# Kernel optimization log

Measured on AMD Instinct MI355X. Metric: run time of the kernel, lower is better.

Reference implementation:

```python
import jax, jax.numpy as jnp
import numpy as np

N_NODES = 50000
N_EDGES = 625000
DIM = 128
DROPOUT_P = 0.5


def setup_inputs() -> dict:
    key = jax.random.key(0)
    kx, ke, kw, kb = jax.random.split(key, 4)
    x = jax.random.normal(kx, (N_NODES, DIM), dtype=jnp.float32)
    edge_index = jax.random.randint(ke, (2, N_EDGES), 0, N_NODES, dtype=jnp.int64)
    # GCNConv linear weight (glorot-ish) and bias
    W = jax.random.normal(kw, (DIM, DIM), dtype=jnp.float32) / np.sqrt(DIM)
    b = jnp.zeros((DIM,), dtype=jnp.float32)
    return {"x": x, "edge_index": edge_index, "W": W, "b": b}


def reference(x, edge_index, W, b):
    N = x.shape[0]
    # --- add self-loops ---
    loop = jnp.arange(N, dtype=edge_index.dtype)
    src = jnp.concatenate([edge_index[0], loop])  # [E+N]
    dst = jnp.concatenate([edge_index[1], loop])  # [E+N]
    # --- symmetric normalization: deg computed on destination nodes ---
    deg = jax.ops.segment_sum(jnp.ones_like(src, dtype=x.dtype), dst, num_segments=N)
    dis = jnp.where(deg > 0, jax.lax.rsqrt(jnp.where(deg > 0, deg, 1.0)), 0.0)
    norm = dis[src] * dis[dst]  # [E+N]
    # --- linear transform, gather, scatter-add ---
    h = x @ W  # [N, D]
    msg = h[src] * norm[:, None]  # [E+N, D]
    out = jax.ops.segment_sum(msg, dst, num_segments=N) + b  # [N, D]
    # --- ReLU + dropout (training mode, fixed key) + residual ---
    out = jax.nn.relu(out)
    keep = jax.random.bernoulli(jax.random.key(42), 1.0 - DROPOUT_P, out.shape)
    out = jnp.where(keep, out / (1.0 - DROPOUT_P), 0.0)
    out = out + x  # residual: input_dim == output_dim
    return out
```

## Files before the change

### kernel.cpp

```cpp
#include <hip/hip_runtime.h>
#include <hip/hip_bf16.h>
#include <stdint.h>

#define NDIM 128
#define LDK 136
#define BSH 9
#define NB_A 1024
#define BCAP 9216

typedef __attribute__((ext_vector_type(8))) short bf16x8;
typedef __attribute__((ext_vector_type(4))) float f32x4;

__device__ __forceinline__ unsigned short f2bf(float f) {
    unsigned u = __float_as_uint(f);
    unsigned r = u + 0x7fffu + ((u >> 16) & 1u);
    return (unsigned short)(r >> 16);
}
__device__ __forceinline__ float bf2f(unsigned short s) {
    return __uint_as_float(((unsigned)s) << 16);
}

__device__ __forceinline__ void load_edge(const unsigned* __restrict__ w, int is64, int E,
                                          int e, int& s, int& d) {
    if (is64) {
        s = (int)w[(size_t)2 * e];
        d = (int)w[(size_t)2 * E + (size_t)2 * e];
    } else {
        s = (int)w[e];
        d = (int)w[(size_t)E + e];
    }
}

__global__ void detect_kernel(const unsigned* __restrict__ w, int* flag) {
    __shared__ int any_nonzero;
    if (threadIdx.x == 0) any_nonzero = 0;
    __syncthreads();
    int nz = 0;
    for (int k = threadIdx.x; k < 2048; k += 256) {
        if (w[2 * k + 1] != 0u) nz = 1;
    }
    if (nz) atomicOr(&any_nonzero, 1);
    __syncthreads();
    if (threadIdx.x == 0) *flag = any_nonzero ? 0 : 1;
}

__global__ __launch_bounds__(256) void hist_kernel(const unsigned* __restrict__ w,
                                                   const int* __restrict__ flag,
                                                   int* __restrict__ hist,
                                                   int E, int nbuck, int chunk) {
    __shared__ int h[128];
    int t = threadIdx.x;
    if (t < 128) h[t] = 0;
    __syncthreads();
    int is64 = *flag;
    int lo = blockIdx.x * chunk;
    int hi = lo + chunk; if (hi > E) hi = E;
    for (int e = lo + t; e < hi; e += 256) {
        int s, d; load_edge(w, is64, E, e, s, d);
        atomicAdd(&h[d >> BSH], 1);
    }
    __syncthreads();
    if (t < nbuck) hist[(size_t)t * gridDim.x + blockIdx.x] = h[t];
}

__global__ __launch_bounds__(1024) void scanhist_kernel(int* __restrict__ hist,
                                                        int* __restrict__ btot, int NB) {
    __shared__ int s[1024];
    int t = threadIdx.x;
    size_t base = (size_t)blockIdx.x * NB;
    int v = hist[base + t];
    s[t] = v;
    __syncthreads();
    for (int d = 1; d < 1024; d <<= 1) {
        int add = (t >= d) ? s[t - d] : 0;
        __syncthreads();
        s[t] += add;
        __syncthreads();
    }
    hist[base + t] = s[t] - v;
    if (t == 1023) btot[blockIdx.x] = s[1023];
}

__global__ __launch_bounds__(128) void scanbuck_kernel(const int* __restrict__ btot,
                                                       int* __restrict__ bbase, int nbuck,
                                                       int* __restrict__ off, int N, int E) {
    __shared__ int s[128];
    int t = threadIdx.x;
    int v = (t < nbuck) ? btot[t] : 0;
    s[t] = v;
    __syncthreads();
    for (int d = 1; d < 128; d <<= 1) {
        int add = (t >= d) ? s[t - d] : 0;
        __syncthreads();
        s[t] += add;
        __syncthreads();
    }
    if (t < nbuck) bbase[t] = s[t] - v;
    if (t == 0) off[N] = E;
}

__global__ __launch_bounds__(256) void bucket_kernel(const unsigned* __restrict__ w,
                                                     const int* __restrict__ flag,
                                                     const int* __restrict__ hist,
                                                     const int* __restrict__ bbase,
                                                     unsigned* __restrict__ ebuf,
                                                     int E, int nbuck, int chunk) {
    __shared__ int cur[128];
    int t = threadIdx.x;
    if (t < nbuck) cur[t] = bbase[t] + hist[(size_t)t * gridDim.x + blockIdx.x];
    __syncthreads();
    int is64 = *flag;
    int lo = blockIdx.x * chunk;
    int hi = lo + chunk; if (hi > E) hi = E;
    for (int e = lo + t; e < hi; e += 256) {
        int s, d; load_edge(w, is64, E, e, s, d);
        int b = d >> BSH;
        int p = atomicAdd(&cur[b], 1);
        ebuf[p] = ((unsigned)s << BSH) | (unsigned)(d & ((1 << BSH) - 1));
    }
}

__global__ __launch_bounds__(512) void csr_kernel(const unsigned* __restrict__ ebuf,
                                                  const int* __restrict__ bbase,
                                                  const int* __restrict__ btot,
                                                  int* __restrict__ adj,
                                                  int* __restrict__ off,
                                                  float* __restrict__ dis,
                                                  int N) {
    __shared__ int lcnt[512];
    __shared__ int lscan[512];
    __shared__ int cur[512];
    __shared__ int tile[BCAP];
    int b = blockIdx.x, t = threadIdx.x;
    int start = bbase[b], cnt = btot[b];
    lcnt[t] = 0;
    __syncthreads();
    for (int i = t; i < cnt; i += 512) atomicAdd(&lcnt[ebuf[start + i] & 511], 1);
    __syncthreads();
    int v = lcnt[t];
    lscan[t] = v;
    __syncthreads();
    for (int d = 1; d < 512; d <<= 1) {
        int add = (t >= d) ? lscan[t - d] : 0;
        __syncthreads();
        lscan[t] += add;
        __syncthreads();
    }
    int ex = lscan[t] - v;
    int node = (b << BSH) + t;
    if (node < N) {
        off[node] = start + ex;
        dis[node] = rsqrtf((float)(v + 1));
    }
    cur[t] = ex;
    __syncthreads();
    if (cnt <= BCAP) {
        for (int i = t; i < cnt; i += 512) {
            unsigned wo = ebuf[start + i];
            int p = atomicAdd(&cur[wo & 511], 1);
            tile[p] = (int)(wo >> BSH);
        }
        __syncthreads();
        for (int i = t; i < cnt; i += 512) adj[start + i] = tile[i];
    } else {
        for (int i = t; i < cnt; i += 512) {
            unsigned wo = ebuf[start + i];
            int p = atomicAdd(&cur[wo & 511], 1);
            adj[start + p] = (int)(wo >> BSH);
        }
    }
}

__global__ __launch_bounds__(256) void gemm_kernel(const float* __restrict__ x,
                                                   const float* __restrict__ W,
                                                   const float* __restrict__ dis,
                                                   unsigned short* __restrict__ hp,
                                                   int N, int ntiles) {
    __shared__ unsigned short Wt[NDIM][LDK];
    int tid = threadIdx.x;
    for (int i = tid; i < NDIM * NDIM; i += 256) {
        int k = i >> 7, c = i & 127;
        Wt[c][k] = f2bf(W[i]);
    }
    __syncthreads();

    const int lane = tid & 63;
    const int wv = tid >> 6;
    const int l15 = lane & 15;
    const int kg = lane >> 4;

    for (int tile = blockIdx.x; tile < ntiles; tile += gridDim.x) {
        const int rowbase = tile * 64 + wv * 16;
        const int arow = rowbase + l15;

        bf16x8 a[4];
#pragma unroll
        for (int s = 0; s < 4; ++s) {
            bf16x8 tt;
            if (arow < N) {
                const float* p = x + (size_t)arow * NDIM + s * 32 + kg * 8;
                float4 f0 = *(const float4*)p;
                float4 f1 = *(const float4*)(p + 4);
                tt[0] = (short)f2bf(f0.x); tt[1] = (short)f2bf(f0.y);
                tt[2] = (short)f2bf(f0.z); tt[3] = (short)f2bf(f0.w);
                tt[4] = (short)f2bf(f1.x); tt[5] = (short)f2bf(f1.y);
                tt[6] = (short)f2bf(f1.z); tt[7] = (short)f2bf(f1.w);
            } else {
#pragma unroll
                for (int e = 0; e < 8; ++e) tt[e] = 0;
            }
            a[s] = tt;
        }

        f32x4 acc[8];
#pragma unroll
        for (int ct = 0; ct < 8; ++ct) acc[ct] = (f32x4){0.f, 0.f, 0.f, 0.f};

#pragma unroll
        for (int ct = 0; ct < 8; ++ct) {
#pragma unroll
            for (int s = 0; s < 4; ++s) {
                bf16x8 bb = *(const bf16x8*)&Wt[ct * 16 + l15][s * 32 + kg * 8];
                acc[ct] = __builtin_amdgcn_mfma_f32_16x16x32_bf16(a[s], bb, acc[ct], 0, 0, 0);
            }
        }

        const int r0 = rowbase + kg * 4;
        float dv[4];
#pragma unroll
        for (int j = 0; j < 4; ++j) dv[j] = (r0 + j < N) ? dis[r0 + j] : 0.f;
#pragma unroll
        for (int ct = 0; ct < 8; ++ct) {
            int col = ct * 16 + l15;
#pragma unroll
            for (int j = 0; j < 4; ++j) {
                int r = r0 + j;
                if (r < N) hp[(size_t)r * NDIM + col] = f2bf(acc[ct][j] * dv[j]);
            }
        }
    }
}

__device__ __forceinline__ unsigned rotl32(unsigned v, int d) {
    return (v << d) | (v >> (32 - d));
}
__device__ __forceinline__ unsigned tf_bits(unsigned ctr) {
    unsigned x0 = 0u, x1 = ctr;
    const unsigned ks0 = 0u, ks1 = 42u, ks2 = 0u ^ 42u ^ 0x1BD11BDAu;
    x0 += ks0; x1 += ks1;
#define RND(r) { x0 += x1; x1 = rotl32(x1, (r)); x1 ^= x0; }
    RND(13) RND(15) RND(26) RND(6)   x0 += ks1; x1 += ks2 + 1u;
    RND(17) RND(29) RND(16) RND(24)  x0 += ks2; x1 += ks0 + 2u;
    RND(13) RND(15) RND(26) RND(6)   x0 += ks0; x1 += ks1 + 3u;
    RND(17) RND(29) RND(16) RND(24)  x0 += ks1; x1 += ks2 + 4u;
    RND(13) RND(15) RND(26) RND(6)   x0 += ks2; x1 += ks0 + 5u;
#undef RND
    return x0 ^ x1;
}

__global__ __launch_bounds__(256) void gather_kernel(const unsigned short* __restrict__ hp,
                                                     const float* __restrict__ x,
                                                     const int* __restrict__ off,
                                                     const int* __restrict__ adj,
                                                     const float* __restrict__ dis,
                                                     const float* __restrict__ b,
                                                     float* __restrict__ out, int N) {
    int wid = (int)((blockIdx.x * 256u + threadIdx.x) >> 6);
    int lane = threadIdx.x & 63;
    int half = lane >> 5;
    int l32 = lane & 31;
    int node = wid * 2 + half;
    bool valid = node < N;
    int nodec = valid ? node : N - 1;
    const float dn = dis[nodec];
    const int c0 = l32 * 4;
    const unsigned short* hpc = hp + c0;

    unsigned ctr = (unsigned)(nodec * NDIM + c0);
    unsigned bt0 = tf_bits(ctr);
    unsigned bt1 = tf_bits(ctr + 1u);
    unsigned bt2 = tf_bits(ctr + 2u);
    unsigned bt3 = tf_bits(ctr + 3u);

    uint2 hv = *(const uint2*)(hpc + (size_t)nodec * NDIM);
    float a00 = bf2f((unsigned short)hv.x), a01 = bf2f((unsigned short)(hv.x >> 16));
    float a02 = bf2f((unsigned short)hv.y), a03 = bf2f((unsigned short)(hv.y >> 16));
    float a10 = 0.f, a11 = 0.f, a12 = 0.f, a13 = 0.f;
    float a20 = 0.f, a21 = 0.f, a22 = 0.f, a23 = 0.f;
    float a30 = 0.f, a31 = 0.f, a32 = 0.f, a33 = 0.f;

    int k0 = valid ? off[nodec] : 0;
    int k1 = valid ? off[nodec + 1] : 0;
    int kb = k0;
    const int sbase = half << 5;
    while (kb < k1) {
        int nb = k1 - kb; if (nb > 32) nb = 32;
        int myadj = (kb + l32 < k1) ? adj[kb + l32] : 0;
        int j = 0;
        for (; j + 4 <= nb; j += 4) {
            int s0 = __shfl(myadj, sbase + j);
            int s1 = __shfl(myadj, sbase + j + 1);
            int s2 = __shfl(myadj, sbase + j + 2);
            int s3 = __shfl(myadj, sbase + j + 3);
            uint2 v0 = *(const uint2*)(hpc + (size_t)s0 * NDIM);
            uint2 v1 = *(const uint2*)(hpc + (size_t)s1 * NDIM);
            uint2 v2 = *(const uint2*)(hpc + (size_t)s2 * NDIM);
            uint2 v3 = *(const uint2*)(hpc + (size_t)s3 * NDIM);
            a00 += bf2f((unsigned short)v0.x); a01 += bf2f((unsigned short)(v0.x >> 16));
            a02 += bf2f((unsigned short)v0.y); a03 += bf2f((unsigned short)(v0.y >> 16));
            a10 += bf2f((unsigned short)v1.x); a11 += bf2f((unsigned short)(v1.x >> 16));
            a12 += bf2f((unsigned short)v1.y); a13 += bf2f((unsigned short)(v1.y >> 16));
            a20 += bf2f((unsigned short)v2.x); a21 += bf2f((unsigned short)(v2.x >> 16));
            a22 += bf2f((unsigned short)v2.y); a23 += bf2f((unsigned short)(v2.y >> 16));
            a30 += bf2f((unsigned short)v3.x); a31 += bf2f((unsigned short)(v3.x >> 16));
            a32 += bf2f((unsigned short)v3.y); a33 += bf2f((unsigned short)(v3.y >> 16));
        }
        for (; j < nb; ++j) {
            int s = __shfl(myadj, sbase + j);
            uint2 v = *(const uint2*)(hpc + (size_t)s * NDIM);
            a00 += bf2f((unsigned short)v.x); a01 += bf2f((unsigned short)(v.x >> 16));
            a02 += bf2f((unsigned short)v.y); a03 += bf2f((unsigned short)(v.y >> 16));
        }
        kb += nb;
    }

    float c0s = (a00 + a10) + (a20 + a30);
    float c1s = (a01 + a11) + (a21 + a31);
    float c2s = (a02 + a12) + (a22 + a32);
    float c3s = (a03 + a13) + (a23 + a33);

    float4 bb = *(const float4*)(b + c0);
    float v0 = fmaxf(fmaf(dn, c0s, bb.x), 0.f);
    float v1 = fmaxf(fmaf(dn, c1s, bb.y), 0.f);
    float v2 = fmaxf(fmaf(dn, c2s, bb.z), 0.f);
    float v3 = fmaxf(fmaf(dn, c3s, bb.w), 0.f);

    v0 = (bt0 >> 31) ? 0.f : v0 * 2.f;
    v1 = (bt1 >> 31) ? 0.f : v1 * 2.f;
    v2 = (bt2 >> 31) ? 0.f : v2 * 2.f;
    v3 = (bt3 >> 31) ? 0.f : v3 * 2.f;

    if (valid) {
        float4 xr = *(const float4*)(x + (size_t)node * NDIM + c0);
        float4 o;
        o.x = v0 + xr.x; o.y = v1 + xr.y; o.z = v2 + xr.z; o.w = v3 + xr.w;
        *(float4*)(out + (size_t)node * NDIM + c0) = o;
    }
}

extern "C" void kernel_launch(void* const* d_in, const int* in_sizes, int n_in,
                              void* d_out, int out_size, void* d_ws, size_t ws_size,
                              hipStream_t stream) {
    const float* x = (const float*)d_in[0];
    const unsigned* edge_w = (const unsigned*)d_in[1];
    const float* W = (const float*)d_in[2];
    const float* b = (const float*)d_in[3];
    float* out = (float*)d_out;

    const int N = in_sizes[0] / NDIM;
    const int E = in_sizes[1] / 2;
    const int nbuck = (N + (1 << BSH) - 1) >> BSH;
    const int chunk = (E + NB_A - 1) / NB_A;
    const int ntiles = (N + 63) / 64;

    char* ws = (char*)d_ws;
    unsigned short* hp = (unsigned short*)ws;
    float* dis   = (float*)(ws + (size_t)N * NDIM * sizeof(short));
    int*   off   = (int*)((char*)dis + (size_t)N * sizeof(float));
    int*   adj   = (int*)((char*)off + (size_t)(N + 4) * sizeof(int));
    unsigned* ebuf = (unsigned*)((char*)adj + (size_t)E * sizeof(int));
    int*   hist  = (int*)((char*)ebuf + (size_t)E * sizeof(unsigned));
    int*   btot  = (int*)((char*)hist + (size_t)128 * NB_A * sizeof(int));
    int*   bbase = (int*)((char*)btot + (size_t)128 * sizeof(int));
    int*   flag  = (int*)((char*)bbase + (size_t)128 * sizeof(int));

    detect_kernel<<<1, 256, 0, stream>>>(edge_w, flag);
    hist_kernel<<<NB_A, 256, 0, stream>>>(edge_w, flag, hist, E, nbuck, chunk);
    scanhist_kernel<<<nbuck, 1024, 0, stream>>>(hist, btot, NB_A);
    scanbuck_kernel<<<1, 128, 0, stream>>>(btot, bbase, nbuck, off, N, E);
    bucket_kernel<<<NB_A, 256, 0, stream>>>(edge_w, flag, hist, bbase, ebuf, E, nbuck, chunk);
    csr_kernel<<<nbuck, 512, 0, stream>>>(ebuf, bbase, btot, adj, off, dis, N);

    gemm_kernel<<<391, 256, 0, stream>>>(x, W, dis, hp, N, ntiles);

    int waves = (N + 1) / 2;
    gather_kernel<<<(waves + 3) / 4, 256, 0, stream>>>(hp, x, off, adj, dis, b, out, N);
}
```

Measured before the change: 84.65 us.

## Fuse detect and bucket-scan kernels, pre-convert W, unroll gather by eight

```diff
diff --git a/kernel.cpp b/kernel.cpp
--- a/kernel.cpp
+++ b/kernel.cpp
@@ -31,30 +31,37 @@
     }
 }
 
-__global__ void detect_kernel(const unsigned* __restrict__ w, int* flag) {
-    __shared__ int any_nonzero;
-    if (threadIdx.x == 0) any_nonzero = 0;
-    __syncthreads();
-    int nz = 0;
-    for (int k = threadIdx.x; k < 2048; k += 256) {
-        if (w[2 * k + 1] != 0u) nz = 1;
-    }
-    if (nz) atomicOr(&any_nonzero, 1);
-    __syncthreads();
-    if (threadIdx.x == 0) *flag = any_nonzero ? 0 : 1;
+__device__ __forceinline__ int detect_is64(const unsigned* __restrict__ w,
+                                           int lo, int hi, int E, int t, int* nzflag) {
+    if (t == 0) *nzflag = 0;
+    __syncthreads();
+    int k = lo + t;
+    if (k < hi && w[2 * (size_t)k + 1] != 0u) atomicOr(nzflag, 1);
+    __syncthreads();
+    return *nzflag ? 0 : 1;
 }
 
 __global__ __launch_bounds__(256) void hist_kernel(const unsigned* __restrict__ w,
-                                                   const int* __restrict__ flag,
+                                                   const float* __restrict__ W,
+                                                   unsigned short* __restrict__ WbfT,
                                                    int* __restrict__ hist,
+                                                   int* __restrict__ lock,
                                                    int E, int nbuck, int chunk) {
     __shared__ int h[128];
+    __shared__ int nzflag;
     int t = threadIdx.x;
     if (t < 128) h[t] = 0;
-    __syncthreads();
-    int is64 = *flag;
+    if (t == 0 && blockIdx.x == 0) *lock = 0;
     int lo = blockIdx.x * chunk;
     int hi = lo + chunk; if (hi > E) hi = E;
+    int is64 = detect_is64(w, lo, hi, E, t, &nzflag);
+
+    if (blockIdx.x < 64) {
+        int idx = blockIdx.x * 256 + t;
+        int k = idx >> 7, c = idx & 127;
+        WbfT[c * 128 + k] = f2bf(W[idx]);
+    }
+
     for (int e = lo + t; e < hi; e += 256) {
         int s, d; load_edge(w, is64, E, e, s, d);
         atomicAdd(&h[d >> BSH], 1);
@@ -64,9 +71,15 @@
 }
 
 __global__ __launch_bounds__(1024) void scanhist_kernel(int* __restrict__ hist,
-                                                        int* __restrict__ btot, int NB) {
+                                                        int* __restrict__ btot,
+                                                        int* __restrict__ bbase,
+                                                        int* __restrict__ off,
+                                                        int* __restrict__ lock,
+                                                        int NB, int nbuck, int N, int E) {
     __shared__ int s[1024];
+    __shared__ int amlast;
     int t = threadIdx.x;
+    if (t == 0) amlast = 0;
     size_t base = (size_t)blockIdx.x * NB;
     int v = hist[base + t];
     s[t] = v;
@@ -78,40 +91,40 @@
         __syncthreads();
     }
     hist[base + t] = s[t] - v;
-    if (t == 1023) btot[blockIdx.x] = s[1023];
-}
-
-__global__ __launch_bounds__(128) void scanbuck_kernel(const int* __restrict__ btot,
-                                                       int* __restrict__ bbase, int nbuck,
-                                                       int* __restrict__ off, int N, int E) {
-    __shared__ int s[128];
-    int t = threadIdx.x;
-    int v = (t < nbuck) ? btot[t] : 0;
-    s[t] = v;
-    __syncthreads();
-    for (int d = 1; d < 128; d <<= 1) {
-        int add = (t >= d) ? s[t - d] : 0;
-        __syncthreads();
-        s[t] += add;
-        __syncthreads();
-    }
-    if (t < nbuck) bbase[t] = s[t] - v;
-    if (t == 0) off[N] = E;
+    if (t == 1023) {
+        atomicExch(&btot[blockIdx.x], s[1023]);
+        __threadfence();
+        int prev = atomicAdd(lock, 1);
+        amlast = (prev == nbuck - 1) ? 1 : 0;
+    }
+    __syncthreads();
+    if (amlast) {
+        int v2 = (t < nbuck) ? atomicAdd(&btot[t], 0) : 0;
+        s[t] = v2;
+        __syncthreads();
+        for (int d = 1; d < 128; d <<= 1) {
+            int add = (t >= d && t < 128) ? s[t - d] : 0;
+            __syncthreads();
+            if (t < 128) s[t] += add;
+            __syncthreads();
+        }
+        if (t < nbuck) bbase[t] = s[t] - v2;
+        if (t == 0) off[N] = E;
+    }
 }
 
 __global__ __launch_bounds__(256) void bucket_kernel(const unsigned* __restrict__ w,
-                                                     const int* __restrict__ flag,
                                                      const int* __restrict__ hist,
                                                      const int* __restrict__ bbase,
                                                      unsigned* __restrict__ ebuf,
                                                      int E, int nbuck, int chunk) {
     __shared__ int cur[128];
+    __shared__ int nzflag;
     int t = threadIdx.x;
     if (t < nbuck) cur[t] = bbase[t] + hist[(size_t)t * gridDim.x + blockIdx.x];
-    __syncthreads();
-    int is64 = *flag;
     int lo = blockIdx.x * chunk;
     int hi = lo + chunk; if (hi > E) hi = E;
+    int is64 = detect_is64(w, lo, hi, E, t, &nzflag);
     for (int e = lo + t; e < hi; e += 256) {
         int s, d; load_edge(w, is64, E, e, s, d);
         int b = d >> BSH;
@@ -172,71 +185,69 @@
 }
 
 __global__ __launch_bounds__(256) void gemm_kernel(const float* __restrict__ x,
-                                                   const float* __restrict__ W,
+                                                   const unsigned short* __restrict__ WbfT,
                                                    const float* __restrict__ dis,
-                                                   unsigned short* __restrict__ hp,
-                                                   int N, int ntiles) {
+                                                   unsigned short* __restrict__ hp, int N) {
     __shared__ unsigned short Wt[NDIM][LDK];
     int tid = threadIdx.x;
-    for (int i = tid; i < NDIM * NDIM; i += 256) {
-        int k = i >> 7, c = i & 127;
-        Wt[c][k] = f2bf(W[i]);
+    for (int ch = tid; ch < 2048; ch += 256) {
+        int c = ch >> 4;
+        int k8 = (ch & 15) << 3;
+        bf16x8 v = *(const bf16x8*)(WbfT + c * 128 + k8);
+        *(bf16x8*)&Wt[c][k8] = v;
     }
     __syncthreads();
 
     const int lane = tid & 63;
     const int wv = tid >> 6;
+    const int rowbase = blockIdx.x * 64 + wv * 16;
     const int l15 = lane & 15;
     const int kg = lane >> 4;
-
-    for (int tile = blockIdx.x; tile < ntiles; tile += gridDim.x) {
-        const int rowbase = tile * 64 + wv * 16;
-        const int arow = rowbase + l15;
-
-        bf16x8 a[4];
+    const int arow = rowbase + l15;
+
+    bf16x8 a[4];
+#pragma unroll
+    for (int s = 0; s < 4; ++s) {
+        bf16x8 tt;
+        if (arow < N) {
+            const float* p = x + (size_t)arow * NDIM + s * 32 + kg * 8;
+            float4 f0 = *(const float4*)p;
+            float4 f1 = *(const float4*)(p + 4);
+            tt[0] = (short)f2bf(f0.x); tt[1] = (short)f2bf(f0.y);
+            tt[2] = (short)f2bf(f0.z); tt[3] = (short)f2bf(f0.w);
+            tt[4] = (short)f2bf(f1.x); tt[5] = (short)f2bf(f1.y);
+            tt[6] = (short)f2bf(f1.z); tt[7] = (short)f2bf(f1.w);
+        } else {
+#pragma unroll
+            for (int e = 0; e < 8; ++e) tt[e] = 0;
+        }
+        a[s] = tt;
+    }
+
+    f32x4 acc[8];
+#pragma unroll
+    for (int ct = 0; ct < 8; ++ct) acc[ct] = (f32x4){0.f, 0.f, 0.f, 0.f};
+
+#pragma unroll
+    for (int ct = 0; ct < 8; ++ct) {
 #pragma unroll
         for (int s = 0; s < 4; ++s) {
-            bf16x8 tt;
-            if (arow < N) {
-                const float* p = x + (size_t)arow * NDIM + s * 32 + kg * 8;
-                float4 f0 = *(const float4*)p;
-                float4 f1 = *(const float4*)(p + 4);
-                tt[0] = (short)f2bf(f0.x); tt[1] = (short)f2bf(f0.y);
-                tt[2] = (short)f2bf(f0.z); tt[3] = (short)f2bf(f0.w);
-                tt[4] = (short)f2bf(f1.x); tt[5] = (short)f2bf(f1.y);
-                tt[6] = (short)f2bf(f1.z); tt[7] = (short)f2bf(f1.w);
-            } else {
-#pragma unroll
-                for (int e = 0; e < 8; ++e) tt[e] = 0;
-            }
-            a[s] = tt;
-        }
-
-        f32x4 acc[8];
-#pragma unroll
-        for (int ct = 0; ct < 8; ++ct) acc[ct] = (f32x4){0.f, 0.f, 0.f, 0.f};
-
-#pragma unroll
-        for (int ct = 0; ct < 8; ++ct) {
-#pragma unroll
-            for (int s = 0; s < 4; ++s) {
-                bf16x8 bb = *(const bf16x8*)&Wt[ct * 16 + l15][s * 32 + kg * 8];
-                acc[ct] = __builtin_amdgcn_mfma_f32_16x16x32_bf16(a[s], bb, acc[ct], 0, 0, 0);
-            }
-        }
-
-        const int r0 = rowbase + kg * 4;
-        float dv[4];
-#pragma unroll
-        for (int j = 0; j < 4; ++j) dv[j] = (r0 + j < N) ? dis[r0 + j] : 0.f;
-#pragma unroll
-        for (int ct = 0; ct < 8; ++ct) {
-            int col = ct * 16 + l15;
-#pragma unroll
-            for (int j = 0; j < 4; ++j) {
-                int r = r0 + j;
-                if (r < N) hp[(size_t)r * NDIM + col] = f2bf(acc[ct][j] * dv[j]);
-            }
+            bf16x8 bb = *(const bf16x8*)&Wt[ct * 16 + l15][s * 32 + kg * 8];
+            acc[ct] = __builtin_amdgcn_mfma_f32_16x16x32_bf16(a[s], bb, acc[ct], 0, 0, 0);
+        }
+    }
+
+    const int r0 = rowbase + kg * 4;
+    float dv[4];
+#pragma unroll
+    for (int j = 0; j < 4; ++j) dv[j] = (r0 + j < N) ? dis[r0 + j] : 0.f;
+#pragma unroll
+    for (int ct = 0; ct < 8; ++ct) {
+        int col = ct * 16 + l15;
+#pragma unroll
+        for (int j = 0; j < 4; ++j) {
+            int r = r0 + j;
+            if (r < N) hp[(size_t)r * NDIM + col] = f2bf(acc[ct][j] * dv[j]);
         }
     }
 }
@@ -297,7 +308,41 @@
         int nb = k1 - kb; if (nb > 32) nb = 32;
         int myadj = (kb + l32 < k1) ? adj[kb + l32] : 0;
         int j = 0;
-        for (; j + 4 <= nb; j += 4) {
+        for (; j + 8 <= nb; j += 8) {
+            int s0 = __shfl(myadj, sbase + j);
+            int s1 = __shfl(myadj, sbase + j + 1);
+            int s2 = __shfl(myadj, sbase + j + 2);
+            int s3 = __shfl(myadj, sbase + j + 3);
+            int s4 = __shfl(myadj, sbase + j + 4);
+            int s5 = __shfl(myadj, sbase + j + 5);
+            int s6 = __shfl(myadj, sbase + j + 6);
+            int s7 = __shfl(myadj, sbase + j + 7);
+            uint2 v0 = *(const uint2*)(hpc + (size_t)s0 * NDIM);
+            uint2 v1 = *(const uint2*)(hpc + (size_t)s1 * NDIM);
+            uint2 v2 = *(const uint2*)(hpc + (size_t)s2 * NDIM);
+            uint2 v3 = *(const uint2*)(hpc + (size_t)s3 * NDIM);
+            uint2 v4 = *(const uint2*)(hpc + (size_t)s4 * NDIM);
+            uint2 v5 = *(const uint2*)(hpc + (size_t)s5 * NDIM);
+            uint2 v6 = *(const uint2*)(hpc + (size_t)s6 * NDIM);
+            uint2 v7 = *(const uint2*)(hpc + (size_t)s7 * NDIM);
+            a00 += bf2f((unsigned short)v0.x); a01 += bf2f((unsigned short)(v0.x >> 16));
+            a02 += bf2f((unsigned short)v0.y); a03 += bf2f((unsigned short)(v0.y >> 16));
+            a10 += bf2f((unsigned short)v1.x); a11 += bf2f((unsigned short)(v1.x >> 16));
+            a12 += bf2f((unsigned short)v1.y); a13 += bf2f((unsigned short)(v1.y >> 16));
+            a20 += bf2f((unsigned short)v2.x); a21 += bf2f((unsigned short)(v2.x >> 16));
+            a22 += bf2f((unsigned short)v2.y); a23 += bf2f((unsigned short)(v2.y >> 16));
+            a30 += bf2f((unsigned short)v3.x); a31 += bf2f((unsigned short)(v3.x >> 16));
+            a32 += bf2f((unsigned short)v3.y); a33 += bf2f((unsigned short)(v3.y >> 16));
+            a00 += bf2f((unsigned short)v4.x); a01 += bf2f((unsigned short)(v4.x >> 16));
+            a02 += bf2f((unsigned short)v4.y); a03 += bf2f((unsigned short)(v4.y >> 16));
+            a10 += bf2f((unsigned short)v5.x); a11 += bf2f((unsigned short)(v5.x >> 16));
+            a12 += bf2f((unsigned short)v5.y); a13 += bf2f((unsigned short)(v5.y >> 16));
+            a20 += bf2f((unsigned short)v6.x); a21 += bf2f((unsigned short)(v6.x >> 16));
+            a22 += bf2f((unsigned short)v6.y); a23 += bf2f((unsigned short)(v6.y >> 16));
+            a30 += bf2f((unsigned short)v7.x); a31 += bf2f((unsigned short)(v7.x >> 16));
+            a32 += bf2f((unsigned short)v7.y); a33 += bf2f((unsigned short)(v7.y >> 16));
+        }
+        if (j + 4 <= nb) {
             int s0 = __shfl(myadj, sbase + j);
             int s1 = __shfl(myadj, sbase + j + 1);
             int s2 = __shfl(myadj, sbase + j + 2);
@@ -314,6 +359,7 @@
             a22 += bf2f((unsigned short)v2.y); a23 += bf2f((unsigned short)(v2.y >> 16));
             a30 += bf2f((unsigned short)v3.x); a31 += bf2f((unsigned short)(v3.x >> 16));
             a32 += bf2f((unsigned short)v3.y); a33 += bf2f((unsigned short)(v3.y >> 16));
+            j += 4;
         }
         for (; j < nb; ++j) {
             int s = __shfl(myadj, sbase + j);
@@ -361,7 +407,6 @@
     const int E = in_sizes[1] / 2;
     const int nbuck = (N + (1 << BSH) - 1) >> BSH;
     const int chunk = (E + NB_A - 1) / NB_A;
-    const int ntiles = (N + 63) / 64;
 
     char* ws = (char*)d_ws;
     unsigned short* hp = (unsigned short*)ws;
@@ -372,16 +417,15 @@
     int*   hist  = (int*)((char*)ebuf + (size_t)E * sizeof(unsigned));
     int*   btot  = (int*)((char*)hist + (size_t)128 * NB_A * sizeof(int));
     int*   bbase = (int*)((char*)btot + (size_t)128 * sizeof(int));
-    int*   flag  = (int*)((char*)bbase + (size_t)128 * sizeof(int));
-
-    detect_kernel<<<1, 256, 0, stream>>>(edge_w, flag);
-    hist_kernel<<<NB_A, 256, 0, stream>>>(edge_w, flag, hist, E, nbuck, chunk);
-    scanhist_kernel<<<nbuck, 1024, 0, stream>>>(hist, btot, NB_A);
-    scanbuck_kernel<<<1, 128, 0, stream>>>(btot, bbase, nbuck, off, N, E);
-    bucket_kernel<<<NB_A, 256, 0, stream>>>(edge_w, flag, hist, bbase, ebuf, E, nbuck, chunk);
+    int*   lock  = (int*)((char*)bbase + (size_t)128 * sizeof(int));
+    unsigned short* WbfT = (unsigned short*)((char*)lock + 64);
+
+    hist_kernel<<<NB_A, 256, 0, stream>>>(edge_w, W, WbfT, hist, lock, E, nbuck, chunk);
+    scanhist_kernel<<<nbuck, 1024, 0, stream>>>(hist, btot, bbase, off, lock, NB_A, nbuck, N, E);
+    bucket_kernel<<<NB_A, 256, 0, stream>>>(edge_w, hist, bbase, ebuf, E, nbuck, chunk);
     csr_kernel<<<nbuck, 512, 0, stream>>>(ebuf, bbase, btot, adj, off, dis, N);
 
-    gemm_kernel<<<391, 256, 0, stream>>>(x, W, dis, hp, N, ntiles);
+    gemm_kernel<<<(N + 63) / 64, 256, 0, stream>>>(x, WbfT, dis, hp, N);
 
     int waves = (N + 1) / 2;
     gather_kernel<<<(waves + 3) / 4, 256, 0, stream>>>(hp, x, off, adj, dis, b, out, N);
```

Measured after the change: 78.31 us. -7.5%, faster.
